# Kernel tuning notes

Hardware: AMD Instinct MI355X
Metric: run time of the kernel (lower is better)

## Reference

```python
import jax, jax.numpy as jnp
import numpy as np

D_MODEL = 1024
H = 16
HEAD = D_MODEL // H  # 64


def setup_inputs() -> dict:
    key = jax.random.key(0)
    ks = jax.random.split(key, 10)
    B, S = 2, 2048
    x = jax.random.normal(ks[0], (B, S, D_MODEL), dtype=jnp.float32)
    y = jax.random.normal(ks[1], (B, S, D_MODEL), dtype=jnp.float32)
    mask = jnp.ones((B, S, S), dtype=jnp.float32)
    s = 1.0 / np.sqrt(D_MODEL)
    Wq = jax.random.normal(ks[2], (D_MODEL, D_MODEL), dtype=jnp.float32) * s
    Wk = jax.random.normal(ks[3], (D_MODEL, D_MODEL), dtype=jnp.float32) * s
    Wv = jax.random.normal(ks[4], (D_MODEL, D_MODEL), dtype=jnp.float32) * s
    Wo = jax.random.normal(ks[5], (D_MODEL, D_MODEL), dtype=jnp.float32) * s
    bq = jnp.zeros((D_MODEL,), jnp.float32)
    bk = jnp.zeros((D_MODEL,), jnp.float32)
    bv = jnp.zeros((D_MODEL,), jnp.float32)
    bo = jnp.zeros((D_MODEL,), jnp.float32)
    return {"x": x, "y": y, "mask": mask, "Wq": Wq, "bq": bq, "Wk": Wk,
            "bk": bk, "Wv": Wv, "bv": bv, "Wo": Wo, "bo": bo}


def reference(x, y, mask, Wq, bq, Wk, bk, Wv, bv, Wo, bo):
    # torch Linear: out = in @ W.T + b; here W stored as [out, in]
    B, Sq, D = x.shape
    Skv = y.shape[1]
    q = x @ Wq.T + bq  # [B, Sq, D]
    k = y @ Wk.T + bk  # [B, Skv, D]
    v = y @ Wv.T + bv
    # chunk(h, dim=-1) + cat(dim=0) == split feature dim into heads (head-major)
    q = q.reshape(B, Sq, H, HEAD)
    k = k.reshape(B, Skv, H, HEAD)
    v = v.reshape(B, Skv, H, HEAD)
    score = jnp.einsum('bqhd,bkhd->bhqk', q, k) / np.sqrt(HEAD)
    score = score + (1.0 - mask[:, None, :, :]) * -1e9
    attn = jax.nn.softmax(score, axis=-1)
    out = jnp.einsum('bhqk,bkhd->bqhd', attn, v).reshape(B, Sq, D)
    return out @ Wo.T + bo
```

## Files before the change

### kernel.cpp

```cpp
#include <hip/hip_runtime.h>
#include <cstdint>
#include <cstddef>

typedef __bf16 bf16x8 __attribute__((ext_vector_type(8)));
typedef float f32x4 __attribute__((ext_vector_type(4)));
typedef unsigned short u16;
typedef unsigned short u16x8 __attribute__((ext_vector_type(8)));
typedef unsigned int u32;

typedef __attribute__((address_space(1))) void gvoid_t;
typedef __attribute__((address_space(3))) void lvoid_t;

__device__ __forceinline__ void gld_lds16(const void* g, void* l) {
  __builtin_amdgcn_global_load_lds((gvoid_t*)g, (lvoid_t*)l, 16, 0, 0);
}

__device__ __forceinline__ u16 f2bf(float f) {
  u32 u = __float_as_uint(f);
  u += 0x7fffu + ((u >> 16) & 1u);
  return (u16)(u >> 16);
}
__device__ __forceinline__ u32 pack2bf(float a, float b) {
  return (u32)f2bf(a) | ((u32)f2bf(b) << 16);
}
__device__ __forceinline__ bf16x8 ld_frag(const u16* p) {
  return __builtin_bit_cast(bf16x8, *(const uint4*)p);
}
__device__ __forceinline__ f32x4 mfma16(bf16x8 a, bf16x8 b, f32x4 c) {
  return __builtin_amdgcn_mfma_f32_16x16x32_bf16(a, b, c, 0, 0, 0);
}
__device__ __forceinline__ float ex2(float x) {
  return __builtin_amdgcn_exp2f(x);
}
__device__ __forceinline__ int swz(int row) { return (row ^ (row >> 3)) & 7; }

#define D_MODEL 1024
#define SEQ     2048
#define NHEAD   16
#define QSC     0.1803368801f
#define MBIAS   (-1.4426950408e9f)

__global__ __launch_bounds__(256) void cvt_kernel(
    const float* __restrict__ x,  const float* __restrict__ y,
    const float* __restrict__ wq, const float* __restrict__ wk,
    const float* __restrict__ wv, const float* __restrict__ wo,
    u16* __restrict__ xb, u16* __restrict__ yb,
    u16* __restrict__ wqb, u16* __restrict__ wkb,
    u16* __restrict__ wvb, u16* __restrict__ wob) {
  const int t = blockIdx.y;
  const float* src;
  u16* dst;
  int n;
  float sc = 1.0f;
  if (t == 0)      { src = x;  dst = xb;  n = 4096 * 1024; }
  else if (t == 1) { src = y;  dst = yb;  n = 4096 * 1024; }
  else if (t == 2) { src = wq; dst = wqb; n = 1024 * 1024; sc = QSC; }
  else if (t == 3) { src = wk; dst = wkb; n = 1024 * 1024; }
  else if (t == 4) { src = wv; dst = wvb; n = 1024 * 1024; }
  else             { src = wo; dst = wob; n = 1024 * 1024; }
  const int i = (blockIdx.x * 256 + threadIdx.x) * 8;
  if (i >= n) return;
  const float4 a = *(const float4*)(src + i);
  const float4 b = *(const float4*)(src + i + 4);
  ushort4 lo, hi;
  lo.x = f2bf(a.x * sc); lo.y = f2bf(a.y * sc); lo.z = f2bf(a.z * sc); lo.w = f2bf(a.w * sc);
  hi.x = f2bf(b.x * sc); hi.y = f2bf(b.y * sc); hi.z = f2bf(b.z * sc); hi.w = f2bf(b.w * sc);
  *(ushort4*)(dst + i) = lo;
  *(ushort4*)(dst + i + 4) = hi;
}

__global__ __launch_bounds__(256) void maskT_kernel(
    const float* __restrict__ mask, u16* __restrict__ biasT) {
  const int kt = blockIdx.x, qt = blockIdx.y, b = blockIdx.z;
  const int tid = threadIdx.x;
  __shared__ u16 Lt[64 * 72];
  const int r = tid >> 2;
  const int cb = (tid & 3) * 16;
  const float* mp = mask + ((size_t)(b * SEQ + qt * 64 + r)) * SEQ + kt * 64 + cb;
#pragma unroll
  for (int j = 0; j < 16; j += 4) {
    const float4 m4 = *(const float4*)(mp + j);
    Lt[(cb + j + 0) * 72 + r] = f2bf((1.0f - m4.x) * MBIAS);
    Lt[(cb + j + 1) * 72 + r] = f2bf((1.0f - m4.y) * MBIAS);
    Lt[(cb + j + 2) * 72 + r] = f2bf((1.0f - m4.z) * MBIAS);
    Lt[(cb + j + 3) * 72 + r] = f2bf((1.0f - m4.w) * MBIAS);
  }
  __syncthreads();
  u16 v[16];
#pragma unroll
  for (int j = 0; j < 16; ++j) v[j] = Lt[r * 72 + cb + j];
  u16* op = biasT + ((size_t)(b * SEQ + kt * 64 + r)) * SEQ + qt * 64 + cb;
  *(uint4*)op = *(const uint4*)v;
  *(uint4*)(op + 8) = *(const uint4*)(v + 8);
}

__global__ __launch_bounds__(256) void vT_kernel(
    const u16* __restrict__ vbuf, u16* __restrict__ vt) {
  const int st = blockIdx.x, h = blockIdx.y, b = blockIdx.z;
  const int tid = threadIdx.x;
  __shared__ u16 Lt[64 * 72];
  const int r = tid >> 2;
  const int cb = (tid & 3) * 16;
  const u16* ip = vbuf + ((size_t)(b * SEQ + st * 64 + r)) * D_MODEL + h * 64 + cb;
  uint4 a0 = *(const uint4*)ip;
  uint4 a1 = *(const uint4*)(ip + 8);
#pragma unroll
  for (int j = 0; j < 8; ++j) {
    Lt[(cb + j) * 72 + r]     = ((const u16*)&a0)[j];
    Lt[(cb + 8 + j) * 72 + r] = ((const u16*)&a1)[j];
  }
  __syncthreads();
  u16 v[16];
#pragma unroll
  for (int j = 0; j < 16; ++j) v[j] = Lt[r * 72 + cb + j];
  u16* op = vt + ((size_t)((b * NHEAD + h) * 64 + r)) * SEQ + st * 64 + cb;
  *(uint4*)op = *(const uint4*)v;
  *(uint4*)(op + 8) = *(const uint4*)(v + 8);
}

template <typename OT>
__device__ __forceinline__ void gemm_block_128(const u16* __restrict__ A,
                                               const u16* __restrict__ W,
                                               const float* __restrict__ bias,
                                               float bscale,
                                               OT* __restrict__ D,
                                               int mb, int nb) {
  __shared__ __align__(16) u16 Asl[128 * 32];
  __shared__ __align__(16) u16 Bsl[128 * 32];
  const int tid = threadIdx.x;
  const int w = tid >> 6, lane = tid & 63, quad = lane >> 4, l16 = lane & 15;
  const int wm = (w & 1) * 64, wn = (w >> 1) * 64;
  const int cidx = w * 64 + lane;

  f32x4 acc[4][4];
#pragma unroll
  for (int i = 0; i < 4; ++i)
#pragma unroll
    for (int j = 0; j < 4; ++j) acc[i][j] = f32x4{0.f, 0.f, 0.f, 0.f};

  for (int k0 = 0; k0 < 1024; k0 += 32) {
    __syncthreads();
#pragma unroll
    for (int t = 0; t < 2; ++t) {
      const int idx = t * 256 + cidx;
      const int row = idx >> 2;
      const int col = (idx & 3) * 8;
      gld_lds16(A + (size_t)(mb * 128 + row) * 1024 + k0 + col,
                (char*)Asl + (size_t)(t * 4 + w) * 1024);
      gld_lds16(W + (size_t)(nb * 128 + row) * 1024 + k0 + col,
                (char*)Bsl + (size_t)(t * 4 + w) * 1024);
    }
    __syncthreads();

    bf16x8 af[4], bfr[4];
#pragma unroll
    for (int i = 0; i < 4; ++i) {
      af[i]  = ld_frag(Asl + (wm + i * 16 + l16) * 32 + quad * 8);
      bfr[i] = ld_frag(Bsl + (wn + i * 16 + l16) * 32 + quad * 8);
    }
#pragma unroll
    for (int i = 0; i < 4; ++i)
#pragma unroll
      for (int j = 0; j < 4; ++j) acc[i][j] = mfma16(af[i], bfr[j], acc[i][j]);
  }

#pragma unroll
  for (int i = 0; i < 4; ++i)
#pragma unroll
    for (int j = 0; j < 4; ++j) {
      const int gn = nb * 128 + wn + j * 16 + l16;
      const float bv = bias[gn] * bscale;
#pragma unroll
      for (int r = 0; r < 4; ++r) {
        const int gm = mb * 128 + wm + i * 16 + quad * 4 + r;
        const float v = acc[i][j][r] + bv;
        if constexpr (sizeof(OT) == 2)
          D[(size_t)gm * 1024 + gn] = (OT)f2bf(v);
        else
          D[(size_t)gm * 1024 + gn] = (OT)v;
      }
    }
}

__global__ __launch_bounds__(256) void qkv_kernel(
    const u16* __restrict__ xb, const u16* __restrict__ yb,
    const u16* __restrict__ Wqb, const u16* __restrict__ Wkb, const u16* __restrict__ Wvb,
    const float* __restrict__ bq, const float* __restrict__ bk, const float* __restrict__ bv,
    u16* __restrict__ qb, u16* __restrict__ kb, u16* __restrict__ vb) {
  const int mat = blockIdx.y >> 3;
  const int nb = blockIdx.y & 7;
  const int mb = blockIdx.x;
  const u16 *A, *W;
  const float* bias;
  u16* D;
  float bscale = 1.0f;
  if (mat == 0)      { A = xb; W = Wqb; bias = bq; D = qb; bscale = QSC; }
  else if (mat == 1) { A = yb; W = Wkb; bias = bk; D = kb; }
  else               { A = yb; W = Wvb; bias = bv; D = vb; }
  gemm_block_128<u16>(A, W, bias, bscale, D, mb, nb);
}

__global__ __launch_bounds__(256) void oproj_kernel(
    const u16* __restrict__ ctx, const u16* __restrict__ Wob,
    const float* __restrict__ bo, float* __restrict__ out) {
  gemm_block_128<float>(ctx, Wob, bo, 1.0f, out, blockIdx.x, blockIdx.y);
}

__global__ __launch_bounds__(256) void attn_kernel(
    const u16* __restrict__ qb, const u16* __restrict__ kb,
    const u16* __restrict__ vt, const u16* __restrict__ biasT,
    u16* __restrict__ ctx) {
  const int h = blockIdx.x;
  const int qblk = blockIdx.y;
  const int b = blockIdx.z;
  const int tid = threadIdx.x, w = tid >> 6, lane = tid & 63;
  const int quad = lane >> 4, l16 = lane & 15;
  const int q0 = qblk * 64;

  __shared__ __align__(16) u16 Ks[64 * 64];
  __shared__ __align__(16) u16 Vs[64 * 64];
  __shared__ __align__(16) u16 Bs[64 * 64];
  __shared__ __align__(16) u16 Ps[4 * 16 * 64];

  const int qrow = q0 + w * 16 + l16;
  const u16* qp = qb + (size_t)(b * SEQ + qrow) * D_MODEL + h * 64;
  const bf16x8 qf0 = ld_frag(qp + quad * 8);
  const bf16x8 qf1 = ld_frag(qp + 32 + quad * 8);

  bf16x8 onesf;
  {
    u16x8 t;
    const u16 ov = (l16 == 0) ? (u16)0x3F80 : (u16)0;
#pragma unroll
    for (int j = 0; j < 8; ++j) t[j] = ov;
    onesf = __builtin_bit_cast(bf16x8, t);
  }

  f32x4 O[4];
#pragma unroll
  for (int dt = 0; dt < 4; ++dt) O[dt] = f32x4{0.f, 0.f, 0.f, 0.f};
  f32x4 O4 = f32x4{0.f, 0.f, 0.f, 0.f};

  const int cidx = w * 64 + lane;
  const int bchunk = w * 2 + (quad >> 1);
  const int boff = (quad & 1) * 4;

  for (int kt = 0; kt < 32; ++kt) {
    const int kv0 = kt * 64;

    __syncthreads();

#pragma unroll
    for (int t = 0; t < 2; ++t) {
      const int idx = t * 256 + cidx;
      const int row = idx >> 3;
      const int g = (idx & 7) ^ swz(row);
      const size_t dst = (size_t)(t * 4 + w) * 1024;
      gld_lds16(kb + (size_t)(b * SEQ + kv0 + row) * D_MODEL + h * 64 + g * 8,
                (char*)Ks + dst);
      gld_lds16(vt + ((size_t)((b * NHEAD + h) * 64 + row)) * SEQ + kv0 + g * 8,
                (char*)Vs + dst);
      gld_lds16(biasT + ((size_t)(b * SEQ + kv0 + row)) * SEQ + q0 + g * 8,
                (char*)Bs + dst);
    }
    __syncthreads();

    u16* Pw = Ps + w * 1024;
#pragma unroll
    for (int nt = 0; nt < 4; ++nt) {
      const int kvl = nt * 16 + l16;
      const u16* bp = Bs + kvl * 64 + ((bchunk ^ swz(kvl)) << 3) + boff;
      const uint2 bw = *(const uint2*)bp;
      f32x4 z;
      z[0] = __uint_as_float(bw.x << 16);
      z[1] = __uint_as_float(bw.x & 0xffff0000u);
      z[2] = __uint_as_float(bw.y << 16);
      z[3] = __uint_as_float(bw.y & 0xffff0000u);
      const bf16x8 kf0 = ld_frag(Ks + kvl * 64 + ((quad       ^ swz(kvl)) * 8));
      const bf16x8 kf1 = ld_frag(Ks + kvl * 64 + (((4 + quad) ^ swz(kvl)) * 8));
      z = mfma16(qf0, kf0, z);
      z = mfma16(qf1, kf1, z);
      const u32 p01 = pack2bf(ex2(z[0]), ex2(z[1]));
      const u32 p23 = pack2bf(ex2(z[2]), ex2(z[3]));
      const int col = nt * 16 + l16;
      const int ch = col >> 3;
      const int cw = col & 7;
      const int pr = quad * 4;
      Pw[(pr + 0) * 64 + ((ch ^ swz(pr + 0)) * 8) + cw] = (u16)p01;
      Pw[(pr + 1) * 64 + ((ch ^ swz(pr + 1)) * 8) + cw] = (u16)(p01 >> 16);
      Pw[(pr + 2) * 64 + ((ch ^ swz(pr + 2)) * 8) + cw] = (u16)p23;
      Pw[(pr + 3) * 64 + ((ch ^ swz(pr + 3)) * 8) + cw] = (u16)(p23 >> 16);
    }
    const bf16x8 pf0 = ld_frag(Pw + l16 * 64 + ((quad       ^ swz(l16)) * 8));
    const bf16x8 pf1 = ld_frag(Pw + l16 * 64 + (((4 + quad) ^ swz(l16)) * 8));

#pragma unroll
    for (int dt = 0; dt < 4; ++dt) {
      const int row = dt * 16 + l16;
      const bf16x8 vf0 = ld_frag(Vs + row * 64 + ((quad       ^ swz(row)) * 8));
      const bf16x8 vf1 = ld_frag(Vs + row * 64 + (((4 + quad) ^ swz(row)) * 8));
      O[dt] = mfma16(pf0, vf0, O[dt]);
      O[dt] = mfma16(pf1, vf1, O[dt]);
    }
    O4 = mfma16(pf0, onesf, O4);
    O4 = mfma16(pf1, onesf, O4);
  }

  float inv[4];
#pragma unroll
  for (int r = 0; r < 4; ++r) {
    const float l = __shfl(O4[r], lane & 48, 64);
    inv[r] = 1.0f / l;
  }

#pragma unroll
  for (int dt = 0; dt < 4; ++dt)
#pragma unroll
    for (int r = 0; r < 4; ++r) {
      const int gq = b * SEQ + q0 + w * 16 + quad * 4 + r;
      const int gd = h * 64 + dt * 16 + l16;
      ctx[(size_t)gq * D_MODEL + gd] = f2bf(O[dt][r] * inv[r]);
    }
}

extern "C" void kernel_launch(void* const* d_in, const int* in_sizes, int n_in,
                              void* d_out, int out_size, void* d_ws, size_t ws_size,
                              hipStream_t stream) {
  (void)in_sizes; (void)n_in; (void)out_size; (void)ws_size;
  const float* x    = (const float*)d_in[0];
  const float* y    = (const float*)d_in[1];
  const float* mask = (const float*)d_in[2];
  const float* Wq   = (const float*)d_in[3];
  const float* bq   = (const float*)d_in[4];
  const float* Wk   = (const float*)d_in[5];
  const float* bk   = (const float*)d_in[6];
  const float* Wv   = (const float*)d_in[7];
  const float* bv   = (const float*)d_in[8];
  const float* Wo   = (const float*)d_in[9];
  const float* bo   = (const float*)d_in[10];
  float* out = (float*)d_out;

  const size_t M4 = (size_t)4096 * 1024;
  const size_t M1 = (size_t)1024 * 1024;
  u16* qbuf  = (u16*)d_ws;
  u16* kbuf  = qbuf + M4;
  u16* vt    = kbuf + M4;
  u16* vbuf  = vt + M4;
  u16* cbuf  = vbuf;
  u16* wob   = vbuf + M4;
  u16* xb    = wob + M1;
  u16* yb    = xb + M4;
  u16* wqb   = yb + M4;
  u16* wkb   = wqb + M1;
  u16* wvb   = wkb + M1;
  u16* biasT = xb;

  cvt_kernel<<<dim3(2048, 6, 1), 256, 0, stream>>>(x, y, Wq, Wk, Wv, Wo,
                                                   xb, yb, wqb, wkb, wvb, wob);
  qkv_kernel<<<dim3(32, 24, 1), 256, 0, stream>>>(xb, yb, wqb, wkb, wvb,
                                                  bq, bk, bv, qbuf, kbuf, vbuf);
  vT_kernel<<<dim3(32, NHEAD, 2), 256, 0, stream>>>(vbuf, vt);
  maskT_kernel<<<dim3(32, 32, 2), 256, 0, stream>>>(mask, biasT);
  attn_kernel<<<dim3(NHEAD, 32, 2), 256, 0, stream>>>(qbuf, kbuf, vt, biasT, cbuf);
  oproj_kernel<<<dim3(32, 8, 1), 256, 0, stream>>>(cbuf, wob, bo, out);
}
```

Before: 273.7 us.

## Enlarge attention Q tile, drop mask transpose, deepen GEMM K-step with swizzle

Attention blocks now cover 128 query rows, with each wave handling two 16-row fragments. This reuses each loaded K/V tile across twice as many queries and halves the number of attention blocks. The transposed-mask kernel is replaced by a plain elementwise bias conversion: QK^T is now computed as K·Q so the score layout matches the row-major bias. The projection GEMMs step K by 64 with an XOR-swizzled LDS layout to halve the barriers per K, and the P pack uses a cheaper round-and-perm conversion. The cost is more LDS and registers per block, which may lower occupancy, and slightly different bf16 rounding of P.

```diff
diff --git a/kernel.cpp b/kernel.cpp
--- a/kernel.cpp
+++ b/kernel.cpp
@@ -20,8 +20,10 @@
   u += 0x7fffu + ((u >> 16) & 1u);
   return (u16)(u >> 16);
 }
-__device__ __forceinline__ u32 pack2bf(float a, float b) {
-  return (u32)f2bf(a) | ((u32)f2bf(b) << 16);
+__device__ __forceinline__ u32 pack_rnd(float a, float b) {
+  const u32 ua = __float_as_uint(a) + 0x8000u;
+  const u32 ub = __float_as_uint(b) + 0x8000u;
+  return __builtin_amdgcn_perm(ub, ua, 0x07060302u);
 }
 __device__ __forceinline__ bf16x8 ld_frag(const u16* p) {
   return __builtin_bit_cast(bf16x8, *(const uint4*)p);
@@ -32,7 +34,6 @@
 __device__ __forceinline__ float ex2(float x) {
   return __builtin_amdgcn_exp2f(x);
 }
-__device__ __forceinline__ int swz(int row) { return (row ^ (row >> 3)) & 7; }
 
 #define D_MODEL 1024
 #define SEQ     2048
@@ -69,29 +70,18 @@
   *(ushort4*)(dst + i + 4) = hi;
 }
 
-__global__ __launch_bounds__(256) void maskT_kernel(
-    const float* __restrict__ mask, u16* __restrict__ biasT) {
-  const int kt = blockIdx.x, qt = blockIdx.y, b = blockIdx.z;
-  const int tid = threadIdx.x;
-  __shared__ u16 Lt[64 * 72];
-  const int r = tid >> 2;
-  const int cb = (tid & 3) * 16;
-  const float* mp = mask + ((size_t)(b * SEQ + qt * 64 + r)) * SEQ + kt * 64 + cb;
-#pragma unroll
-  for (int j = 0; j < 16; j += 4) {
-    const float4 m4 = *(const float4*)(mp + j);
-    Lt[(cb + j + 0) * 72 + r] = f2bf((1.0f - m4.x) * MBIAS);
-    Lt[(cb + j + 1) * 72 + r] = f2bf((1.0f - m4.y) * MBIAS);
-    Lt[(cb + j + 2) * 72 + r] = f2bf((1.0f - m4.z) * MBIAS);
-    Lt[(cb + j + 3) * 72 + r] = f2bf((1.0f - m4.w) * MBIAS);
-  }
-  __syncthreads();
-  u16 v[16];
-#pragma unroll
-  for (int j = 0; j < 16; ++j) v[j] = Lt[r * 72 + cb + j];
-  u16* op = biasT + ((size_t)(b * SEQ + kt * 64 + r)) * SEQ + qt * 64 + cb;
-  *(uint4*)op = *(const uint4*)v;
-  *(uint4*)(op + 8) = *(const uint4*)(v + 8);
+__global__ __launch_bounds__(256) void maskC_kernel(
+    const float* __restrict__ mask, u16* __restrict__ biasC) {
+  const int i = (blockIdx.x * 256 + threadIdx.x) * 8;
+  const float4 a = *(const float4*)(mask + i);
+  const float4 b = *(const float4*)(mask + i + 4);
+  ushort4 lo, hi;
+  lo.x = f2bf(MBIAS - a.x * MBIAS); lo.y = f2bf(MBIAS - a.y * MBIAS);
+  lo.z = f2bf(MBIAS - a.z * MBIAS); lo.w = f2bf(MBIAS - a.w * MBIAS);
+  hi.x = f2bf(MBIAS - b.x * MBIAS); hi.y = f2bf(MBIAS - b.y * MBIAS);
+  hi.z = f2bf(MBIAS - b.z * MBIAS); hi.w = f2bf(MBIAS - b.w * MBIAS);
+  *(ushort4*)(biasC + i) = lo;
+  *(ushort4*)(biasC + i + 4) = hi;
 }
 
 __global__ __launch_bounds__(256) void vT_kernel(
@@ -125,8 +115,8 @@
                                                float bscale,
                                                OT* __restrict__ D,
                                                int mb, int nb) {
-  __shared__ __align__(16) u16 Asl[128 * 32];
-  __shared__ __align__(16) u16 Bsl[128 * 32];
+  __shared__ __align__(16) u16 Asl[128 * 64];
+  __shared__ __align__(16) u16 Bsl[128 * 64];
   const int tid = threadIdx.x;
   const int w = tid >> 6, lane = tid & 63, quad = lane >> 4, l16 = lane & 15;
   const int wm = (w & 1) * 64, wn = (w >> 1) * 64;
@@ -138,30 +128,34 @@
 #pragma unroll
     for (int j = 0; j < 4; ++j) acc[i][j] = f32x4{0.f, 0.f, 0.f, 0.f};
 
-  for (int k0 = 0; k0 < 1024; k0 += 32) {
+  for (int k0 = 0; k0 < 1024; k0 += 64) {
     __syncthreads();
 #pragma unroll
-    for (int t = 0; t < 2; ++t) {
+    for (int t = 0; t < 4; ++t) {
       const int idx = t * 256 + cidx;
-      const int row = idx >> 2;
-      const int col = (idx & 3) * 8;
-      gld_lds16(A + (size_t)(mb * 128 + row) * 1024 + k0 + col,
-                (char*)Asl + (size_t)(t * 4 + w) * 1024);
-      gld_lds16(W + (size_t)(nb * 128 + row) * 1024 + k0 + col,
-                (char*)Bsl + (size_t)(t * 4 + w) * 1024);
+      const int row = idx >> 3;
+      const int g = (idx & 7) ^ (row & 7);
+      const size_t dst = (size_t)(t * 4 + w) * 1024;
+      gld_lds16(A + (size_t)(mb * 128 + row) * 1024 + k0 + g * 8, (char*)Asl + dst);
+      gld_lds16(W + (size_t)(nb * 128 + row) * 1024 + k0 + g * 8, (char*)Bsl + dst);
     }
     __syncthreads();
 
-    bf16x8 af[4], bfr[4];
-#pragma unroll
-    for (int i = 0; i < 4; ++i) {
-      af[i]  = ld_frag(Asl + (wm + i * 16 + l16) * 32 + quad * 8);
-      bfr[i] = ld_frag(Bsl + (wn + i * 16 + l16) * 32 + quad * 8);
-    }
-#pragma unroll
-    for (int i = 0; i < 4; ++i)
-#pragma unroll
-      for (int j = 0; j < 4; ++j) acc[i][j] = mfma16(af[i], bfr[j], acc[i][j]);
+#pragma unroll
+    for (int kk = 0; kk < 2; ++kk) {
+      bf16x8 af[4], bfr[4];
+#pragma unroll
+      for (int i = 0; i < 4; ++i) {
+        const int ar = wm + i * 16 + l16;
+        const int br = wn + i * 16 + l16;
+        af[i]  = ld_frag(Asl + ar * 64 + (((kk * 4 + quad) ^ (ar & 7)) * 8));
+        bfr[i] = ld_frag(Bsl + br * 64 + (((kk * 4 + quad) ^ (br & 7)) * 8));
+      }
+#pragma unroll
+      for (int i = 0; i < 4; ++i)
+#pragma unroll
+        for (int j = 0; j < 4; ++j) acc[i][j] = mfma16(af[i], bfr[j], acc[i][j]);
+    }
   }
 
 #pragma unroll
@@ -208,25 +202,28 @@
 
 __global__ __launch_bounds__(256) void attn_kernel(
     const u16* __restrict__ qb, const u16* __restrict__ kb,
-    const u16* __restrict__ vt, const u16* __restrict__ biasT,
+    const u16* __restrict__ vt, const u16* __restrict__ biasC,
     u16* __restrict__ ctx) {
   const int h = blockIdx.x;
   const int qblk = blockIdx.y;
   const int b = blockIdx.z;
   const int tid = threadIdx.x, w = tid >> 6, lane = tid & 63;
   const int quad = lane >> 4, l16 = lane & 15;
-  const int q0 = qblk * 64;
+  const int q0 = qblk * 128;
 
   __shared__ __align__(16) u16 Ks[64 * 64];
   __shared__ __align__(16) u16 Vs[64 * 64];
-  __shared__ __align__(16) u16 Bs[64 * 64];
-  __shared__ __align__(16) u16 Ps[4 * 16 * 64];
-
-  const int qrow = q0 + w * 16 + l16;
-  const u16* qp = qb + (size_t)(b * SEQ + qrow) * D_MODEL + h * 64;
-  const bf16x8 qf0 = ld_frag(qp + quad * 8);
-  const bf16x8 qf1 = ld_frag(qp + 32 + quad * 8);
-
+  __shared__ __align__(16) u16 Bs[128 * 64];
+  __shared__ __align__(16) u16 Ps[4 * 32 * 64];
+
+  const int qbase = w * 32;
+  bf16x8 qf[2][2];
+#pragma unroll
+  for (int f = 0; f < 2; ++f) {
+    const u16* qp = qb + (size_t)(b * SEQ + q0 + qbase + f * 16 + l16) * D_MODEL + h * 64;
+    qf[f][0] = ld_frag(qp + quad * 8);
+    qf[f][1] = ld_frag(qp + 32 + quad * 8);
+  }
   bf16x8 onesf;
   {
     u16x8 t;
@@ -236,91 +233,108 @@
     onesf = __builtin_bit_cast(bf16x8, t);
   }
 
-  f32x4 O[4];
-#pragma unroll
-  for (int dt = 0; dt < 4; ++dt) O[dt] = f32x4{0.f, 0.f, 0.f, 0.f};
-  f32x4 O4 = f32x4{0.f, 0.f, 0.f, 0.f};
+  f32x4 O[2][4];
+#pragma unroll
+  for (int f = 0; f < 2; ++f)
+#pragma unroll
+    for (int dt = 0; dt < 4; ++dt) O[f][dt] = f32x4{0.f, 0.f, 0.f, 0.f};
+  f32x4 O4[2] = {f32x4{0.f, 0.f, 0.f, 0.f}, f32x4{0.f, 0.f, 0.f, 0.f}};
 
   const int cidx = w * 64 + lane;
-  const int bchunk = w * 2 + (quad >> 1);
-  const int boff = (quad & 1) * 4;
+  u16* Pw = Ps + w * 2048;
 
   for (int kt = 0; kt < 32; ++kt) {
     const int kv0 = kt * 64;
 
     __syncthreads();
-
 #pragma unroll
     for (int t = 0; t < 2; ++t) {
       const int idx = t * 256 + cidx;
       const int row = idx >> 3;
-      const int g = (idx & 7) ^ swz(row);
+      const int g = (idx & 7) ^ (row & 7);
       const size_t dst = (size_t)(t * 4 + w) * 1024;
       gld_lds16(kb + (size_t)(b * SEQ + kv0 + row) * D_MODEL + h * 64 + g * 8,
                 (char*)Ks + dst);
       gld_lds16(vt + ((size_t)((b * NHEAD + h) * 64 + row)) * SEQ + kv0 + g * 8,
                 (char*)Vs + dst);
-      gld_lds16(biasT + ((size_t)(b * SEQ + kv0 + row)) * SEQ + q0 + g * 8,
-                (char*)Bs + dst);
+    }
+#pragma unroll
+    for (int t = 0; t < 4; ++t) {
+      const int idx = t * 256 + cidx;
+      const int row = idx >> 3;
+      const int g = (idx & 7) ^ (row & 7);
+      gld_lds16(biasC + (size_t)(b * SEQ + q0 + row) * SEQ + kv0 + g * 8,
+                (char*)Bs + (size_t)(t * 4 + w) * 1024);
     }
     __syncthreads();
 
-    u16* Pw = Ps + w * 1024;
 #pragma unroll
     for (int nt = 0; nt < 4; ++nt) {
       const int kvl = nt * 16 + l16;
-      const u16* bp = Bs + kvl * 64 + ((bchunk ^ swz(kvl)) << 3) + boff;
-      const uint2 bw = *(const uint2*)bp;
-      f32x4 z;
-      z[0] = __uint_as_float(bw.x << 16);
-      z[1] = __uint_as_float(bw.x & 0xffff0000u);
-      z[2] = __uint_as_float(bw.y << 16);
-      z[3] = __uint_as_float(bw.y & 0xffff0000u);
-      const bf16x8 kf0 = ld_frag(Ks + kvl * 64 + ((quad       ^ swz(kvl)) * 8));
-      const bf16x8 kf1 = ld_frag(Ks + kvl * 64 + (((4 + quad) ^ swz(kvl)) * 8));
-      z = mfma16(qf0, kf0, z);
-      z = mfma16(qf1, kf1, z);
-      const u32 p01 = pack2bf(ex2(z[0]), ex2(z[1]));
-      const u32 p23 = pack2bf(ex2(z[2]), ex2(z[3]));
-      const int col = nt * 16 + l16;
-      const int ch = col >> 3;
-      const int cw = col & 7;
-      const int pr = quad * 4;
-      Pw[(pr + 0) * 64 + ((ch ^ swz(pr + 0)) * 8) + cw] = (u16)p01;
-      Pw[(pr + 1) * 64 + ((ch ^ swz(pr + 1)) * 8) + cw] = (u16)(p01 >> 16);
-      Pw[(pr + 2) * 64 + ((ch ^ swz(pr + 2)) * 8) + cw] = (u16)p23;
-      Pw[(pr + 3) * 64 + ((ch ^ swz(pr + 3)) * 8) + cw] = (u16)(p23 >> 16);
-    }
-    const bf16x8 pf0 = ld_frag(Pw + l16 * 64 + ((quad       ^ swz(l16)) * 8));
-    const bf16x8 pf1 = ld_frag(Pw + l16 * 64 + (((4 + quad) ^ swz(l16)) * 8));
-
+      const bf16x8 kf0 = ld_frag(Ks + kvl * 64 + ((quad ^ (kvl & 7)) * 8));
+      const bf16x8 kf1 = ld_frag(Ks + kvl * 64 + (((4 + quad) ^ (kvl & 7)) * 8));
+#pragma unroll
+      for (int f = 0; f < 2; ++f) {
+        const int br = qbase + f * 16 + l16;
+        const int ck = nt * 2 + (quad >> 1);
+        const uint2 bw = *(const uint2*)(Bs + br * 64 + ((ck ^ (br & 7)) * 8) + (quad & 1) * 4);
+        f32x4 z;
+        z[0] = __uint_as_float(bw.x << 16);
+        z[1] = __uint_as_float(bw.x & 0xffff0000u);
+        z[2] = __uint_as_float(bw.y << 16);
+        z[3] = __uint_as_float(bw.y & 0xffff0000u);
+        z = mfma16(kf0, qf[f][0], z);
+        z = mfma16(kf1, qf[f][1], z);
+        uint2 pv;
+        pv.x = pack_rnd(ex2(z[0]), ex2(z[1]));
+        pv.y = pack_rnd(ex2(z[2]), ex2(z[3]));
+        const int pr = f * 16 + l16;
+        *(uint2*)(Pw + pr * 64 + ((ck ^ (pr & 7)) * 8) + (quad & 1) * 4) = pv;
+      }
+    }
+
+    bf16x8 pf[2][2];
+#pragma unroll
+    for (int f = 0; f < 2; ++f) {
+      const int pr = f * 16 + l16;
+      pf[f][0] = ld_frag(Pw + pr * 64 + ((quad ^ (pr & 7)) * 8));
+      pf[f][1] = ld_frag(Pw + pr * 64 + (((4 + quad) ^ (pr & 7)) * 8));
+    }
 #pragma unroll
     for (int dt = 0; dt < 4; ++dt) {
-      const int row = dt * 16 + l16;
-      const bf16x8 vf0 = ld_frag(Vs + row * 64 + ((quad       ^ swz(row)) * 8));
-      const bf16x8 vf1 = ld_frag(Vs + row * 64 + (((4 + quad) ^ swz(row)) * 8));
-      O[dt] = mfma16(pf0, vf0, O[dt]);
-      O[dt] = mfma16(pf1, vf1, O[dt]);
-    }
-    O4 = mfma16(pf0, onesf, O4);
-    O4 = mfma16(pf1, onesf, O4);
-  }
-
-  float inv[4];
-#pragma unroll
-  for (int r = 0; r < 4; ++r) {
-    const float l = __shfl(O4[r], lane & 48, 64);
-    inv[r] = 1.0f / l;
-  }
-
-#pragma unroll
-  for (int dt = 0; dt < 4; ++dt)
-#pragma unroll
-    for (int r = 0; r < 4; ++r) {
-      const int gq = b * SEQ + q0 + w * 16 + quad * 4 + r;
-      const int gd = h * 64 + dt * 16 + l16;
-      ctx[(size_t)gq * D_MODEL + gd] = f2bf(O[dt][r] * inv[r]);
-    }
+      const int vr = dt * 16 + l16;
+      const bf16x8 vf0 = ld_frag(Vs + vr * 64 + ((quad ^ (vr & 7)) * 8));
+      const bf16x8 vf1 = ld_frag(Vs + vr * 64 + (((4 + quad) ^ (vr & 7)) * 8));
+#pragma unroll
+      for (int f = 0; f < 2; ++f) {
+        O[f][dt] = mfma16(pf[f][0], vf0, O[f][dt]);
+        O[f][dt] = mfma16(pf[f][1], vf1, O[f][dt]);
+      }
+    }
+#pragma unroll
+    for (int f = 0; f < 2; ++f) {
+      O4[f] = mfma16(pf[f][0], onesf, O4[f]);
+      O4[f] = mfma16(pf[f][1], onesf, O4[f]);
+    }
+  }
+
+  float inv[2][4];
+#pragma unroll
+  for (int f = 0; f < 2; ++f)
+#pragma unroll
+    for (int r = 0; r < 4; ++r)
+      inv[f][r] = 1.0f / __shfl(O4[f][r], lane & 48, 64);
+
+#pragma unroll
+  for (int f = 0; f < 2; ++f)
+#pragma unroll
+    for (int dt = 0; dt < 4; ++dt)
+#pragma unroll
+      for (int r = 0; r < 4; ++r) {
+        const int gq = b * SEQ + q0 + qbase + f * 16 + quad * 4 + r;
+        const int gd = h * 64 + dt * 16 + l16;
+        ctx[(size_t)gq * D_MODEL + gd] = f2bf(O[f][dt][r] * inv[f][r]);
+      }
 }
 
 extern "C" void kernel_launch(void* const* d_in, const int* in_sizes, int n_in,
@@ -353,14 +367,14 @@
   u16* wqb   = yb + M4;
   u16* wkb   = wqb + M1;
   u16* wvb   = wkb + M1;
-  u16* biasT = xb;
+  u16* biasC = xb;
 
   cvt_kernel<<<dim3(2048, 6, 1), 256, 0, stream>>>(x, y, Wq, Wk, Wv, Wo,
                                                    xb, yb, wqb, wkb, wvb, wob);
   qkv_kernel<<<dim3(32, 24, 1), 256, 0, stream>>>(xb, yb, wqb, wkb, wvb,
                                                   bq, bk, bv, qbuf, kbuf, vbuf);
   vT_kernel<<<dim3(32, NHEAD, 2), 256, 0, stream>>>(vbuf, vt);
-  maskT_kernel<<<dim3(32, 32, 2), 256, 0, stream>>>(mask, biasT);
-  attn_kernel<<<dim3(NHEAD, 32, 2), 256, 0, stream>>>(qbuf, kbuf, vt, biasT, cbuf);
+  maskC_kernel<<<dim3(4096, 1, 1), 256, 0, stream>>>(mask, biasC);
+  attn_kernel<<<dim3(NHEAD, 16, 2), 256, 0, stream>>>(qbuf, kbuf, vt, biasC, cbuf);
   oproj_kernel<<<dim3(32, 8, 1), 256, 0, stream>>>(cbuf, wob, bo, out);
 }
```

Result: no change. 269.8 us (-1.4%).
